# Kernel optimization log

Hardware: AMD Instinct MI355X
Metric: run time of the kernel (lower is better)

## Reference

```python
import jax, jax.numpy as jnp
import numpy as np

W_L1, W_NORMAL, W_LAPLACIAN = 1.0, 1.0, 0.1
NORM_EPS = 1e-6   # F.normalize eps
COS_EPS = 1e-8    # F.cosine_similarity default eps


def setup_inputs() -> dict:
    key = jax.random.key(0)
    k1, k2, k3, k4, k5, k6 = jax.random.split(key, 6)
    N, F, NNZ = 1_000_000, 2_000_000, 8_000_000
    return {
        "V_rec": jax.random.normal(k1, (N, 3), dtype=jnp.float32),
        "V_gt": jax.random.normal(k2, (N, 3), dtype=jnp.float32),
        "faces": jax.random.randint(k3, (F, 3), 0, N, dtype=jnp.int64)
        if jax.config.jax_enable_x64 else jax.random.randint(k3, (F, 3), 0, N, dtype=jnp.int32),
        "L_rows": jax.random.randint(k4, (NNZ,), 0, N, dtype=jnp.int32),
        "L_cols": jax.random.randint(k5, (NNZ,), 0, N, dtype=jnp.int32),
        "L_vals": jax.random.normal(k6, (NNZ,), dtype=jnp.float32),
    }


def _vertex_normals(verts, faces):
    # gather verts by face indices: [F,3] each
    v0 = verts[faces[:, 0]]
    v1 = verts[faces[:, 1]]
    v2 = verts[faces[:, 2]]
    face_normals = jnp.cross(v1 - v0, v2 - v0)  # [F,3]
    vn = (jnp.zeros_like(verts)
          .at[faces[:, 0]].add(face_normals)
          .at[faces[:, 1]].add(face_normals)
          .at[faces[:, 2]].add(face_normals))
    norm = jnp.linalg.norm(vn, axis=1, keepdims=True)
    return vn / jnp.maximum(norm, NORM_EPS)


def _cosine_sim(a, b):
    dot = jnp.sum(a * b, axis=1)
    na = jnp.linalg.norm(a, axis=1)
    nb = jnp.linalg.norm(b, axis=1)
    return dot / (jnp.maximum(na, COS_EPS) * jnp.maximum(nb, COS_EPS))


def _spmm(rows, cols, vals, V):
    # sparse [N,N] @ dense [N,3] via gather + segment_sum
    return jax.ops.segment_sum(vals[:, None] * V[cols], rows, num_segments=V.shape[0])


def reference(V_rec, V_gt, faces, L_rows, L_cols, L_vals):
    # L1 term
    loss_l1 = jnp.mean(jnp.abs(V_rec - V_gt))
    # Normal cosine term
    normals_gt = _vertex_normals(V_gt, faces)
    normals_rec = _vertex_normals(V_rec, faces)
    cos_n = jnp.nan_to_num(_cosine_sim(normals_rec, normals_gt), nan=1.0)
    loss_normal = jnp.mean(1.0 - cos_n)
    # Laplacian cosine term
    delta_gt = _spmm(L_rows, L_cols, L_vals, V_gt)
    delta_rec = _spmm(L_rows, L_cols, L_vals, V_rec)
    cos_l = jnp.nan_to_num(_cosine_sim(delta_rec, delta_gt), nan=1.0)
    loss_laplacian = jnp.mean(1.0 - cos_l)
    finite = jnp.isfinite(delta_gt).all() & jnp.isfinite(delta_rec).all()
    loss_laplacian = jnp.where(finite, loss_laplacian, 0.0)
    return W_L1 * loss_l1 + W_NORMAL * loss_normal + W_LAPLACIAN * loss_laplacian
```

## Files before the change

### kernel.cpp

```cpp
#include <hip/hip_runtime.h>
#include <hip/hip_bf16.h>

#define NORM_EPS_F 1e-6f
#define COS_EPS_F  1e-8f
#define BK   1024
#define BKSH 10

__device__ __forceinline__ void atomAddF(float* p, float v) {
    unsafeAtomicAdd(p, v);
}

template<int NV>
__device__ __forceinline__ void blockReduceAtomicN(float (&v)[NV], float* dst) {
    #pragma unroll
    for (int off = 32; off > 0; off >>= 1) {
        #pragma unroll
        for (int k = 0; k < NV; ++k) v[k] += __shfl_down(v[k], off, 64);
    }
    __shared__ float red[4][NV];
    int wave = threadIdx.x >> 6, lane = threadIdx.x & 63;
    if (lane == 0) {
        #pragma unroll
        for (int k = 0; k < NV; ++k) red[wave][k] = v[k];
    }
    __syncthreads();
    if (threadIdx.x == 0) {
        float s[NV];
        #pragma unroll
        for (int k = 0; k < NV; ++k) s[k] = 0.f;
        for (int w = 0; w < 4; ++w)
            #pragma unroll
            for (int k = 0; k < NV; ++k) s[k] += red[w][k];
        #pragma unroll
        for (int k = 0; k < NV; ++k) atomAddF(&dst[k], s[k]);
    }
}


__global__ void __launch_bounds__(256) pack_l1_kernel(
    const float* __restrict__ Vr, const float* __restrict__ Vg,
    float4* __restrict__ Vp, float* __restrict__ accum, int N)
{
    int i = blockIdx.x * blockDim.x + threadIdx.x;
    float l1[1] = {0.f};
    if (i < N) {
        float rx = Vr[3 * i], ry = Vr[3 * i + 1], rz = Vr[3 * i + 2];
        float gx = Vg[3 * i], gy = Vg[3 * i + 1], gz = Vg[3 * i + 2];
        Vp[2 * i]     = make_float4(rx, ry, rz, 0.f);
        Vp[2 * i + 1] = make_float4(gx, gy, gz, 0.f);
        l1[0] = fabsf(rx - gx) + fabsf(ry - gy) + fabsf(rz - gz);
    }
    blockReduceAtomicN<1>(l1, &accum[0]);
}

__global__ void __launch_bounds__(256) fn_kernel(
    const float4* __restrict__ Vp, const int* __restrict__ faces,
    float4* __restrict__ FN, int F)
{
    int f = blockIdx.x * blockDim.x + threadIdx.x;
    if (f >= F) return;
    int i0 = faces[3 * f], i1 = faces[3 * f + 1], i2 = faces[3 * f + 2];
    float4 r0 = Vp[2 * i0], r1 = Vp[2 * i1], r2 = Vp[2 * i2];
    float4 g0 = Vp[2 * i0 + 1], g1 = Vp[2 * i1 + 1], g2 = Vp[2 * i2 + 1];
    {
        float ax = r1.x - r0.x, ay = r1.y - r0.y, az = r1.z - r0.z;
        float bx = r2.x - r0.x, by = r2.y - r0.y, bz = r2.z - r0.z;
        FN[2 * f] = make_float4(ay * bz - az * by, az * bx - ax * bz, ax * by - ay * bx, 0.f);
    }
    {
        float ax = g1.x - g0.x, ay = g1.y - g0.y, az = g1.z - g0.z;
        float bx = g2.x - g0.x, by = g2.y - g0.y, bz = g2.z - g0.z;
        FN[2 * f + 1] = make_float4(ay * bz - az * by, az * bx - ax * bz, ax * by - ay * bx, 0.f);
    }
}

__global__ void __launch_bounds__(256) bucket_faces_kernel(
    const int* __restrict__ faces, int* __restrict__ cnt,
    unsigned* __restrict__ recF, int capF, int F, int b0, int bcnt, int chunk)
{
    __shared__ int hist[1024];
    int f0 = blockIdx.x * chunk;
    int f1 = min(f0 + chunk, F);
    for (int b = threadIdx.x; b < bcnt; b += blockDim.x) hist[b] = 0;
    __syncthreads();
    for (int f = f0 + threadIdx.x; f < f1; f += blockDim.x) {
        #pragma unroll
        for (int c = 0; c < 3; ++c) {
            unsigned bb = ((unsigned)faces[3 * f + c] >> BKSH) - (unsigned)b0;
            if (bb < (unsigned)bcnt) atomicAdd(&hist[bb], 1);
        }
    }
    __syncthreads();
    for (int b = threadIdx.x; b < bcnt; b += blockDim.x) {
        int h = hist[b];
        if (h) hist[b] = atomicAdd(&cnt[b], h);
    }
    __syncthreads();
    for (int f = f0 + threadIdx.x; f < f1; f += blockDim.x) {
        #pragma unroll
        for (int c = 0; c < 3; ++c) {
            int vtx = faces[3 * f + c];
            unsigned bb = ((unsigned)vtx >> BKSH) - (unsigned)b0;
            if (bb < (unsigned)bcnt) {
                int pos = atomicAdd(&hist[bb], 1);
                if (pos < capF)
                    recF[(size_t)bb * capF + pos] =
                        ((unsigned)f << BKSH) | (unsigned)(vtx & (BK - 1));
            }
        }
    }
}

__global__ void __launch_bounds__(256) accum_normals_kernel(
    const float4* __restrict__ Vp, const float4* __restrict__ FN,
    const int* __restrict__ faces,
    const int* __restrict__ cnt, const unsigned* __restrict__ recF, int capF,
    float* __restrict__ accum, int N, int b0, int use_fn)
{
    __shared__ float vnr[3 * BK];
    __shared__ float vng[3 * BK];
    int g = blockIdx.x;
    for (int i = threadIdx.x; i < 3 * BK; i += blockDim.x) { vnr[i] = 0.f; vng[i] = 0.f; }
    __syncthreads();

    int n = min(cnt[g], capF);
    for (int i = threadIdx.x; i < n; i += blockDim.x) {
        unsigned rec = recF[(size_t)g * capF + i];
        int lv = rec & (BK - 1);
        int f  = rec >> BKSH;
        float4 nr, ng;
        if (use_fn) {
            nr = FN[2 * f];
            ng = FN[2 * f + 1];
        } else {
            int i0 = faces[3 * f], i1 = faces[3 * f + 1], i2 = faces[3 * f + 2];
            float4 r0 = Vp[2 * i0], r1 = Vp[2 * i1], r2 = Vp[2 * i2];
            float4 g0 = Vp[2 * i0 + 1], g1 = Vp[2 * i1 + 1], g2 = Vp[2 * i2 + 1];
            float ax = r1.x - r0.x, ay = r1.y - r0.y, az = r1.z - r0.z;
            float bx = r2.x - r0.x, by = r2.y - r0.y, bz = r2.z - r0.z;
            nr = make_float4(ay * bz - az * by, az * bx - ax * bz, ax * by - ay * bx, 0.f);
            ax = g1.x - g0.x; ay = g1.y - g0.y; az = g1.z - g0.z;
            bx = g2.x - g0.x; by = g2.y - g0.y; bz = g2.z - g0.z;
            ng = make_float4(ay * bz - az * by, az * bx - ax * bz, ax * by - ay * bx, 0.f);
        }
        atomicAdd(&vnr[3 * lv + 0], nr.x);
        atomicAdd(&vnr[3 * lv + 1], nr.y);
        atomicAdd(&vnr[3 * lv + 2], nr.z);
        atomicAdd(&vng[3 * lv + 0], ng.x);
        atomicAdd(&vng[3 * lv + 1], ng.y);
        atomicAdd(&vng[3 * lv + 2], ng.z);
    }
    __syncthreads();

    float ln[1] = {0.f};
    for (int lv = threadIdx.x; lv < BK; lv += blockDim.x) {
        int gv = ((b0 + g) << BKSH) + lv;
        if (gv < N) {
            float ax = vnr[3 * lv], ay = vnr[3 * lv + 1], az = vnr[3 * lv + 2];
            float bx = vng[3 * lv], by = vng[3 * lv + 1], bz = vng[3 * lv + 2];
            float na = sqrtf(ax * ax + ay * ay + az * az);
            float nb = sqrtf(bx * bx + by * by + bz * bz);
            float ia = 1.0f / fmaxf(na, NORM_EPS_F);
            float ib = 1.0f / fmaxf(nb, NORM_EPS_F);
            ax *= ia; ay *= ia; az *= ia;
            bx *= ib; by *= ib; bz *= ib;
            float dot = ax * bx + ay * by + az * bz;
            float nna = sqrtf(ax * ax + ay * ay + az * az);
            float nnb = sqrtf(bx * bx + by * by + bz * bz);
            float cosn = dot / (fmaxf(nna, COS_EPS_F) * fmaxf(nnb, COS_EPS_F));
            if (isnan(cosn)) cosn = 1.0f;
            ln[0] += 1.0f - cosn;
        }
    }
    blockReduceAtomicN<1>(ln, &accum[1]);
}

__global__ void __launch_bounds__(256) bucket_L_kernel(
    const int* __restrict__ rows, const int* __restrict__ cols,
    const float* __restrict__ vals, int* __restrict__ cnt,
    int2* __restrict__ recL, int capL, int nnz, int b0, int bcnt, int chunk)
{
    __shared__ int hist[1024];
    int i0 = blockIdx.x * chunk;
    int i1 = min(i0 + chunk, nnz);
    for (int b = threadIdx.x; b < bcnt; b += blockDim.x) hist[b] = 0;
    __syncthreads();
    for (int i = i0 + threadIdx.x; i < i1; i += blockDim.x) {
        unsigned bb = ((unsigned)rows[i] >> BKSH) - (unsigned)b0;
        if (bb < (unsigned)bcnt) atomicAdd(&hist[bb], 1);
    }
    __syncthreads();
    for (int b = threadIdx.x; b < bcnt; b += blockDim.x) {
        int h = hist[b];
        if (h) hist[b] = atomicAdd(&cnt[b], h);
    }
    __syncthreads();
    for (int i = i0 + threadIdx.x; i < i1; i += blockDim.x) {
        int r = rows[i];
        unsigned bb = ((unsigned)r >> BKSH) - (unsigned)b0;
        if (bb < (unsigned)bcnt) {
            int pos = atomicAdd(&hist[bb], 1);
            if (pos < capL)
                recL[(size_t)bb * capL + pos] = make_int2(
                    (int)(((unsigned)cols[i] << BKSH) | (unsigned)(r & (BK - 1))),
                    __float_as_int(vals[i]));
        }
    }
}

__global__ void __launch_bounds__(256) accum_lap_kernel(
    const float4* __restrict__ Vp,
    const int* __restrict__ cnt, const int2* __restrict__ recL, int capL,
    float* __restrict__ accum, int N, int b0)
{
    __shared__ float dlr[3 * BK];
    __shared__ float dlg[3 * BK];
    int g = blockIdx.x;
    for (int i = threadIdx.x; i < 3 * BK; i += blockDim.x) { dlr[i] = 0.f; dlg[i] = 0.f; }
    __syncthreads();

    int n = min(cnt[g], capL);
    for (int i = threadIdx.x; i < n; i += blockDim.x) {
        int2 rc = recL[(size_t)g * capL + i];
        unsigned u = (unsigned)rc.x;
        int lv  = u & (BK - 1);
        int col = u >> BKSH;
        float v = __int_as_float(rc.y);
        float4 pr = Vp[2 * col];
        float4 pg = Vp[2 * col + 1];
        atomicAdd(&dlr[3 * lv + 0], v * pr.x);
        atomicAdd(&dlr[3 * lv + 1], v * pr.y);
        atomicAdd(&dlr[3 * lv + 2], v * pr.z);
        atomicAdd(&dlg[3 * lv + 0], v * pg.x);
        atomicAdd(&dlg[3 * lv + 1], v * pg.y);
        atomicAdd(&dlg[3 * lv + 2], v * pg.z);
    }
    __syncthreads();

    float vals2[2] = {0.f, 0.f};
    for (int lv = threadIdx.x; lv < BK; lv += blockDim.x) {
        int gv = ((b0 + g) << BKSH) + lv;
        if (gv < N) {
            float px = dlr[3 * lv], py = dlr[3 * lv + 1], pz = dlr[3 * lv + 2];
            float qx = dlg[3 * lv], qy = dlg[3 * lv + 1], qz = dlg[3 * lv + 2];
            bool fin = isfinite(px) && isfinite(py) && isfinite(pz) &&
                       isfinite(qx) && isfinite(qy) && isfinite(qz);
            vals2[1] += fin ? 0.f : 1.f;
            float dotl = px * qx + py * qy + pz * qz;
            float npn = sqrtf(px * px + py * py + pz * pz);
            float nqn = sqrtf(qx * qx + qy * qy + qz * qz);
            float cosl = dotl / (fmaxf(npn, COS_EPS_F) * fmaxf(nqn, COS_EPS_F));
            if (isnan(cosl)) cosl = 1.0f;
            vals2[0] += 1.0f - cosl;
        }
    }
    blockReduceAtomicN<2>(vals2, &accum[2]);
}

__global__ void finalize_kernel(const float* __restrict__ accum,
                                float* __restrict__ out, int N)
{
    float invN = 1.0f / (float)N;
    float l1 = accum[0] * invN * (1.0f / 3.0f);
    float ln = accum[1] * invN;
    float ll = (accum[3] > 0.0f) ? 0.0f : accum[2] * invN;
    out[0] = 1.0f * l1 + 1.0f * ln + 0.1f * ll;
}


__global__ void __launch_bounds__(256) face_normals_kernel(
    const float* __restrict__ Vr, const float* __restrict__ Vg,
    const int* __restrict__ faces,
    float* __restrict__ vn_rec, float* __restrict__ vn_gt, int F)
{
    int f = blockIdx.x * blockDim.x + threadIdx.x;
    if (f >= F) return;
    int i0 = faces[3 * f + 0], i1 = faces[3 * f + 1], i2 = faces[3 * f + 2];
    {
        float v0x = Vr[3 * i0], v0y = Vr[3 * i0 + 1], v0z = Vr[3 * i0 + 2];
        float v1x = Vr[3 * i1], v1y = Vr[3 * i1 + 1], v1z = Vr[3 * i1 + 2];
        float v2x = Vr[3 * i2], v2y = Vr[3 * i2 + 1], v2z = Vr[3 * i2 + 2];
        float ax = v1x - v0x, ay = v1y - v0y, az = v1z - v0z;
        float bx = v2x - v0x, by = v2y - v0y, bz = v2z - v0z;
        float nx = ay * bz - az * by, ny = az * bx - ax * bz, nz = ax * by - ay * bx;
        atomAddF(&vn_rec[3 * i0], nx); atomAddF(&vn_rec[3 * i0 + 1], ny); atomAddF(&vn_rec[3 * i0 + 2], nz);
        atomAddF(&vn_rec[3 * i1], nx); atomAddF(&vn_rec[3 * i1 + 1], ny); atomAddF(&vn_rec[3 * i1 + 2], nz);
        atomAddF(&vn_rec[3 * i2], nx); atomAddF(&vn_rec[3 * i2 + 1], ny); atomAddF(&vn_rec[3 * i2 + 2], nz);
    }
    {
        float v0x = Vg[3 * i0], v0y = Vg[3 * i0 + 1], v0z = Vg[3 * i0 + 2];
        float v1x = Vg[3 * i1], v1y = Vg[3 * i1 + 1], v1z = Vg[3 * i1 + 2];
        float v2x = Vg[3 * i2], v2y = Vg[3 * i2 + 1], v2z = Vg[3 * i2 + 2];
        float ax = v1x - v0x, ay = v1y - v0y, az = v1z - v0z;
        float bx = v2x - v0x, by = v2y - v0y, bz = v2z - v0z;
        float nx = ay * bz - az * by, ny = az * bx - ax * bz, nz = ax * by - ay * bx;
        atomAddF(&vn_gt[3 * i0], nx); atomAddF(&vn_gt[3 * i0 + 1], ny); atomAddF(&vn_gt[3 * i0 + 2], nz);
        atomAddF(&vn_gt[3 * i1], nx); atomAddF(&vn_gt[3 * i1 + 1], ny); atomAddF(&vn_gt[3 * i1 + 2], nz);
        atomAddF(&vn_gt[3 * i2], nx); atomAddF(&vn_gt[3 * i2 + 1], ny); atomAddF(&vn_gt[3 * i2 + 2], nz);
    }
}

__global__ void __launch_bounds__(256) spmm_kernel(
    const float* __restrict__ Vr, const float* __restrict__ Vg,
    const int* __restrict__ rows, const int* __restrict__ cols,
    const float* __restrict__ vals,
    float* __restrict__ dl_rec, float* __restrict__ dl_gt, int nnz)
{
    int i = blockIdx.x * blockDim.x + threadIdx.x;
    if (i >= nnz) return;
// ... 14 lines not shown
    float* __restrict__ accum, int N)
{
    int i = blockIdx.x * blockDim.x + threadIdx.x;
    float l1 = 0.0f, ln = 0.0f, ll = 0.0f, nonfin = 0.0f;
    if (i < N) {
        float rx = Vr[3 * i], ry = Vr[3 * i + 1], rz = Vr[3 * i + 2];
        float gx = Vg[3 * i], gy = Vg[3 * i + 1], gz = Vg[3 * i + 2];
        l1 = fabsf(rx - gx) + fabsf(ry - gy) + fabsf(rz - gz);
        float ax = vn_rec[3 * i], ay = vn_rec[3 * i + 1], az = vn_rec[3 * i + 2];
        float bx = vn_gt[3 * i],  by = vn_gt[3 * i + 1],  bz = vn_gt[3 * i + 2];
        float na = sqrtf(ax * ax + ay * ay + az * az);
        float nb = sqrtf(bx * bx + by * by + bz * bz);
        float ia = 1.0f / fmaxf(na, NORM_EPS_F);
        float ib = 1.0f / fmaxf(nb, NORM_EPS_F);
        ax *= ia; ay *= ia; az *= ia; bx *= ib; by *= ib; bz *= ib;
        float dot = ax * bx + ay * by + az * bz;
        float nna = sqrtf(ax * ax + ay * ay + az * az);
        float nnb = sqrtf(bx * bx + by * by + bz * bz);
        float cosn = dot / (fmaxf(nna, COS_EPS_F) * fmaxf(nnb, COS_EPS_F));
        if (isnan(cosn)) cosn = 1.0f;
        ln = 1.0f - cosn;
        float px = dl_rec[3 * i], py = dl_rec[3 * i + 1], pz = dl_rec[3 * i + 2];
        float qx = dl_gt[3 * i],  qy = dl_gt[3 * i + 1],  qz = dl_gt[3 * i + 2];
        bool fin = isfinite(px) && isfinite(py) && isfinite(pz) &&
                   isfinite(qx) && isfinite(qy) && isfinite(qz);
        nonfin = fin ? 0.0f : 1.0f;
        float dotl = px * qx + py * qy + pz * qz;
        float npn = sqrtf(px * px + py * py + pz * pz);
        float nqn = sqrtf(qx * qx + qy * qy + qz * qz);
        float cosl = dotl / (fmaxf(npn, COS_EPS_F) * fmaxf(nqn, COS_EPS_F));
        if (isnan(cosl)) cosl = 1.0f;
        ll = 1.0f - cosl;
    }
    float a[1] = {l1};  blockReduceAtomicN<1>(a, &accum[0]);
    float b[1] = {ln};  blockReduceAtomicN<1>(b, &accum[1]);
    float c2[2] = {ll, nonfin}; blockReduceAtomicN<2>(c2, &accum[2]);
}


extern "C" void kernel_launch(void* const* d_in, const int* in_sizes, int n_in,
                              void* d_out, int out_size, void* d_ws, size_t ws_size,
                              hipStream_t stream)
{
    const float* Vr    = (const float*)d_in[0];
    const float* Vg    = (const float*)d_in[1];
    const int*   faces = (const int*)d_in[2];
    const int*   Lr    = (const int*)d_in[3];
    const int*   Lc    = (const int*)d_in[4];
    const float* Lv    = (const float*)d_in[5];

    const int N   = in_sizes[0] / 3;
    const int F   = in_sizes[2] / 3;
    const int NNZ = in_sizes[3];
    const int NB  = (N + BK - 1) >> BKSH;

    float* ws = (float*)d_ws;
    const int B = 256;

    const long long baseW  = 1028;
    const long long vpackW = 8LL * N;
    const long long fnW    = 8LL * F;
    const long long totW   = (long long)(ws_size / 4);

    const int capF = 3 * F / (NB > 0 ? NB : 1) + 1 + 1024;
    const int capL = NNZ / (NB > 0 ? NB : 1) + 1 + 1024;

    long long availA = totW - baseW - vpackW - fnW;
    long long availB = totW - baseW - vpackW;
    bool tierA = availA >= (long long)capF * 64;
    long long availF = tierA ? availA : availB;

    int NBG_F = (int)(availF / capF);
    int NBG_L = (int)(availB / (2LL * capL));
    if (NBG_F > NB) NBG_F = NB;
    if (NBG_L > NB) NBG_L = NB;
    if (NBG_F > 1024) NBG_F = 1024;
    if (NBG_L > 1024) NBG_L = 1024;

    bool fast = (N <= (1 << 20)) && (F <= (1 << 22)) &&
                NBG_F >= 32 && NBG_L >= 32;

    if (fast) {
        float*    accum = ws;
        int*      cnt   = (int*)(ws + 4);
        float4*   Vp    = (float4*)(ws + baseW);
        float4*   FN    = (float4*)(ws + baseW + vpackW);
        unsigned* recF  = (unsigned*)(ws + baseW + vpackW + (tierA ? fnW : 0));
        int2*     recL  = (int2*)(ws + baseW + vpackW);

        hipMemsetAsync(accum, 0, 4 * sizeof(float), stream);

        pack_l1_kernel<<<dim3((N + B - 1) / B), dim3(B), 0, stream>>>(Vr, Vg, Vp, accum, N);
        if (tierA)
            fn_kernel<<<dim3((F + B - 1) / B), dim3(B), 0, stream>>>(Vp, faces, FN, F);

        const int CHF = 4096, CHL = 8192;
        int passF = (NB + NBG_F - 1) / NBG_F;
        for (int p = 0; p < passF; ++p) {
            int b0 = p * NBG_F;
            int bcnt = NB - b0 < NBG_F ? NB - b0 : NBG_F;
            hipMemsetAsync(cnt, 0, (size_t)bcnt * sizeof(int), stream);
            bucket_faces_kernel<<<dim3((F + CHF - 1) / CHF), dim3(B), 0, stream>>>(
                faces, cnt, recF, capF, F, b0, bcnt, CHF);
            accum_normals_kernel<<<dim3(bcnt), dim3(B), 0, stream>>>(
                Vp, FN, faces, cnt, recF, capF, accum, N, b0, tierA ? 1 : 0);
        }
        int passL = (NB + NBG_L - 1) / NBG_L;
        for (int p = 0; p < passL; ++p) {
            int b0 = p * NBG_L;
            int bcnt = NB - b0 < NBG_L ? NB - b0 : NBG_L;
            hipMemsetAsync(cnt, 0, (size_t)bcnt * sizeof(int), stream);
            bucket_L_kernel<<<dim3((NNZ + CHL - 1) / CHL), dim3(B), 0, stream>>>(
                Lr, Lc, Lv, cnt, recL, capL, NNZ, b0, bcnt, CHL);
            accum_lap_kernel<<<dim3(bcnt), dim3(B), 0, stream>>>(
                Vp, cnt, recL, capL, accum, N, b0);
        }
        finalize_kernel<<<dim3(1), dim3(1), 0, stream>>>(accum, (float*)d_out, N);
    } else {
        float* vn_rec = ws;
        float* vn_gt  = ws + (size_t)3 * N;
        float* dl_rec = ws + (size_t)6 * N;
        float* dl_gt  = ws + (size_t)9 * N;
        float* accum  = ws + (size_t)12 * N;
        hipMemsetAsync(d_ws, 0, ((size_t)12 * N + 4) * sizeof(float), stream);
        face_normals_kernel<<<dim3((F + B - 1) / B), dim3(B), 0, stream>>>(Vr, Vg, faces, vn_rec, vn_gt, F);
        spmm_kernel<<<dim3((NNZ + B - 1) / B), dim3(B), 0, stream>>>(Vr, Vg, Lr, Lc, Lv, dl_rec, dl_gt, NNZ);
        reduce_kernel<<<dim3((N + B - 1) / B), dim3(B), 0, stream>>>(Vr, Vg, vn_rec, vn_gt, dl_rec, dl_gt, accum, N);
        finalize_kernel<<<dim3(1), dim3(1), 0, stream>>>(accum, (float*)d_out, N);
    }
}
```

Baseline: 1.102 ms.

## Halve bucket size, batch gathers for memory-level parallelism, two faces per thread

Result: slower. 1.146 ms (+4.0%).

```diff
diff --git a/kernel.cpp b/kernel.cpp
--- a/kernel.cpp
+++ b/kernel.cpp
@@ -3,8 +3,9 @@
 
 #define NORM_EPS_F 1e-6f
 #define COS_EPS_F  1e-8f
-#define BK   1024
-#define BKSH 10
+#define BK   512
+#define BKSH 9
+#define NBGMAX 2048
 
 __device__ __forceinline__ void atomAddF(float* p, float v) {
     unsafeAtomicAdd(p, v);
@@ -57,20 +58,39 @@
     const float4* __restrict__ Vp, const int* __restrict__ faces,
     float4* __restrict__ FN, int F)
 {
-    int f = blockIdx.x * blockDim.x + threadIdx.x;
-    if (f >= F) return;
-    int i0 = faces[3 * f], i1 = faces[3 * f + 1], i2 = faces[3 * f + 2];
-    float4 r0 = Vp[2 * i0], r1 = Vp[2 * i1], r2 = Vp[2 * i2];
-    float4 g0 = Vp[2 * i0 + 1], g1 = Vp[2 * i1 + 1], g2 = Vp[2 * i2 + 1];
-    {
-        float ax = r1.x - r0.x, ay = r1.y - r0.y, az = r1.z - r0.z;
-        float bx = r2.x - r0.x, by = r2.y - r0.y, bz = r2.z - r0.z;
-        FN[2 * f] = make_float4(ay * bz - az * by, az * bx - ax * bz, ax * by - ay * bx, 0.f);
-    }
-    {
-        float ax = g1.x - g0.x, ay = g1.y - g0.y, az = g1.z - g0.z;
-        float bx = g2.x - g0.x, by = g2.y - g0.y, bz = g2.z - g0.z;
-        FN[2 * f + 1] = make_float4(ay * bz - az * by, az * bx - ax * bz, ax * by - ay * bx, 0.f);
+    int half = (F + 1) >> 1;
+    int t = blockIdx.x * blockDim.x + threadIdx.x;
+    if (t >= half) return;
+    int fi[2] = {t, t + half};
+    int n = (fi[1] < F) ? 2 : 1;
+    int idx[2][3];
+    #pragma unroll
+    for (int k = 0; k < 2; ++k) {
+        if (k < n) {
+            idx[k][0] = faces[3 * fi[k]];
+            idx[k][1] = faces[3 * fi[k] + 1];
+            idx[k][2] = faces[3 * fi[k] + 2];
+        }
+    }
+    float4 r0[2], r1[2], r2[2], g0[2], g1[2], g2[2];
+    #pragma unroll
+    for (int k = 0; k < 2; ++k) {
+        if (k < n) {
+            r0[k] = Vp[2 * idx[k][0]]; g0[k] = Vp[2 * idx[k][0] + 1];
+            r1[k] = Vp[2 * idx[k][1]]; g1[k] = Vp[2 * idx[k][1] + 1];
+            r2[k] = Vp[2 * idx[k][2]]; g2[k] = Vp[2 * idx[k][2] + 1];
+        }
+    }
+    #pragma unroll
+    for (int k = 0; k < 2; ++k) {
+        if (k < n) {
+            float ax = r1[k].x - r0[k].x, ay = r1[k].y - r0[k].y, az = r1[k].z - r0[k].z;
+            float bx = r2[k].x - r0[k].x, by = r2[k].y - r0[k].y, bz = r2[k].z - r0[k].z;
+            FN[2 * fi[k]] = make_float4(ay * bz - az * by, az * bx - ax * bz, ax * by - ay * bx, 0.f);
+            ax = g1[k].x - g0[k].x; ay = g1[k].y - g0[k].y; az = g1[k].z - g0[k].z;
+            bx = g2[k].x - g0[k].x; by = g2[k].y - g0[k].y; bz = g2[k].z - g0[k].z;
+            FN[2 * fi[k] + 1] = make_float4(ay * bz - az * by, az * bx - ax * bz, ax * by - ay * bx, 0.f);
+        }
     }
 }
 
@@ -78,7 +98,7 @@
     const int* __restrict__ faces, int* __restrict__ cnt,
     unsigned* __restrict__ recF, int capF, int F, int b0, int bcnt, int chunk)
 {
-    __shared__ int hist[1024];
+    __shared__ int hist[NBGMAX];
     int f0 = blockIdx.x * chunk;
     int f1 = min(f0 + chunk, F);
     for (int b = threadIdx.x; b < bcnt; b += blockDim.x) hist[b] = 0;
@@ -123,11 +143,36 @@
     for (int i = threadIdx.x; i < 3 * BK; i += blockDim.x) { vnr[i] = 0.f; vng[i] = 0.f; }
     __syncthreads();
 
+    const unsigned* rec = recF + (size_t)g * capF;
     int n = min(cnt[g], capF);
-    for (int i = threadIdx.x; i < n; i += blockDim.x) {
-        unsigned rec = recF[(size_t)g * capF + i];
-        int lv = rec & (BK - 1);
-        int f  = rec >> BKSH;
+    int i = threadIdx.x;
+    if (use_fn) {
+        for (; i + 768 < n; i += 1024) {
+            unsigned rc[4];
+            rc[0] = rec[i]; rc[1] = rec[i + 256]; rc[2] = rec[i + 512]; rc[3] = rec[i + 768];
+            float4 nr[4], ng[4];
+            #pragma unroll
+            for (int k = 0; k < 4; ++k) {
+                int f = rc[k] >> BKSH;
+                nr[k] = FN[2 * f];
+                ng[k] = FN[2 * f + 1];
+            }
+            #pragma unroll
+            for (int k = 0; k < 4; ++k) {
+                int lv = rc[k] & (BK - 1);
+                atomicAdd(&vnr[3 * lv + 0], nr[k].x);
+                atomicAdd(&vnr[3 * lv + 1], nr[k].y);
+                atomicAdd(&vnr[3 * lv + 2], nr[k].z);
+                atomicAdd(&vng[3 * lv + 0], ng[k].x);
+                atomicAdd(&vng[3 * lv + 1], ng[k].y);
+                atomicAdd(&vng[3 * lv + 2], ng[k].z);
+            }
+        }
+    }
+    for (; i < n; i += 256) {
+        unsigned rc = rec[i];
+        int lv = rc & (BK - 1);
+        int f  = rc >> BKSH;
         float4 nr, ng;
         if (use_fn) {
             nr = FN[2 * f];
@@ -180,7 +225,7 @@
     const float* __restrict__ vals, int* __restrict__ cnt,
     int2* __restrict__ recL, int capL, int nnz, int b0, int bcnt, int chunk)
 {
-    __shared__ int hist[1024];
+    __shared__ int hist[NBGMAX];
     int i0 = blockIdx.x * chunk;
     int i1 = min(i0 + chunk, nnz);
     for (int b = threadIdx.x; b < bcnt; b += blockDim.x) hist[b] = 0;
@@ -219,9 +264,33 @@
     for (int i = threadIdx.x; i < 3 * BK; i += blockDim.x) { dlr[i] = 0.f; dlg[i] = 0.f; }
     __syncthreads();
 
+    const int2* rec = recL + (size_t)g * capL;
     int n = min(cnt[g], capL);
-    for (int i = threadIdx.x; i < n; i += blockDim.x) {
-        int2 rc = recL[(size_t)g * capL + i];
+    int i = threadIdx.x;
+    for (; i + 768 < n; i += 1024) {
+        int2 rc[4];
+        rc[0] = rec[i]; rc[1] = rec[i + 256]; rc[2] = rec[i + 512]; rc[3] = rec[i + 768];
+        float4 pr[4], pg[4];
+        #pragma unroll
+        for (int k = 0; k < 4; ++k) {
+            int col = (unsigned)rc[k].x >> BKSH;
+            pr[k] = Vp[2 * col];
+            pg[k] = Vp[2 * col + 1];
+        }
+        #pragma unroll
+        for (int k = 0; k < 4; ++k) {
+            int lv = (unsigned)rc[k].x & (BK - 1);
+            float v = __int_as_float(rc[k].y);
+            atomicAdd(&dlr[3 * lv + 0], v * pr[k].x);
+            atomicAdd(&dlr[3 * lv + 1], v * pr[k].y);
+            atomicAdd(&dlr[3 * lv + 2], v * pr[k].z);
+            atomicAdd(&dlg[3 * lv + 0], v * pg[k].x);
+            atomicAdd(&dlg[3 * lv + 1], v * pg[k].y);
+            atomicAdd(&dlg[3 * lv + 2], v * pg[k].z);
+        }
+    }
+    for (; i < n; i += 256) {
+        int2 rc = rec[i];
         unsigned u = (unsigned)rc.x;
         int lv  = u & (BK - 1);
         int col = u >> BKSH;
@@ -380,13 +449,13 @@
     float* ws = (float*)d_ws;
     const int B = 256;
 
-    const long long baseW  = 1028;
+    const long long baseW  = 4 + NBGMAX;
     const long long vpackW = 8LL * N;
     const long long fnW    = 8LL * F;
     const long long totW   = (long long)(ws_size / 4);
 
-    const int capF = 3 * F / (NB > 0 ? NB : 1) + 1 + 1024;
-    const int capL = NNZ / (NB > 0 ? NB : 1) + 1 + 1024;
+    const int capF = 3 * F / (NB > 0 ? NB : 1) + 1 + 640;
+    const int capL = NNZ / (NB > 0 ? NB : 1) + 1 + 640;
 
     long long availA = totW - baseW - vpackW - fnW;
     long long availB = totW - baseW - vpackW;
@@ -397,8 +466,8 @@
     int NBG_L = (int)(availB / (2LL * capL));
     if (NBG_F > NB) NBG_F = NB;
     if (NBG_L > NB) NBG_L = NB;
-    if (NBG_F > 1024) NBG_F = 1024;
-    if (NBG_L > 1024) NBG_L = 1024;
+    if (NBG_F > NBGMAX) NBG_F = NBGMAX;
+    if (NBG_L > NBGMAX) NBG_L = NBGMAX;
 
     bool fast = (N <= (1 << 20)) && (F <= (1 << 22)) &&
                 NBG_F >= 32 && NBG_L >= 32;
@@ -414,8 +483,10 @@
         hipMemsetAsync(accum, 0, 4 * sizeof(float), stream);
 
         pack_l1_kernel<<<dim3((N + B - 1) / B), dim3(B), 0, stream>>>(Vr, Vg, Vp, accum, N);
-        if (tierA)
-            fn_kernel<<<dim3((F + B - 1) / B), dim3(B), 0, stream>>>(Vp, faces, FN, F);
+        if (tierA) {
+            int half = (F + 1) >> 1;
+            fn_kernel<<<dim3((half + B - 1) / B), dim3(B), 0, stream>>>(Vp, faces, FN, F);
+        }
 
         const int CHF = 4096, CHL = 8192;
         int passF = (NB + NBG_F - 1) / NBG_F;
```

## Replace per-pass bucketing with multi-level radix scatter and fp16-packed fat records

Applied to the files above, without the earlier changes.

Measured after the change: 1.394 ms. 26.5% more time.

```diff
diff --git a/kernel.cpp b/kernel.cpp
--- a/kernel.cpp
+++ b/kernel.cpp
@@ -1,13 +1,29 @@
 #include <hip/hip_runtime.h>
 #include <hip/hip_bf16.h>
+#include <hip/hip_fp16.h>
 
 #define NORM_EPS_F 1e-6f
 #define COS_EPS_F  1e-8f
-#define BK   1024
-#define BKSH 10
+#define BK    512
+#define BKSH  9
+#define CRSH  14
+#define K2    32
+#define CH1   4096
+#define CHFS  2048
 
 __device__ __forceinline__ void atomAddF(float* p, float v) {
     unsafeAtomicAdd(p, v);
+}
+
+__device__ __forceinline__ unsigned packh2(float a, float b) {
+    return (unsigned)__half_as_ushort(__float2half(a)) |
+           ((unsigned)__half_as_ushort(__float2half(b)) << 16);
+}
+__device__ __forceinline__ float unpL(int u) {
+    return __half2float(__ushort_as_half((unsigned short)((unsigned)u & 0xffff)));
+}
+__device__ __forceinline__ float unpH(int u) {
+    return __half2float(__ushort_as_half((unsigned short)((unsigned)u >> 16)));
 }
 
 template<int NV>
@@ -53,105 +69,186 @@
     blockReduceAtomicN<1>(l1, &accum[0]);
 }
 
-__global__ void __launch_bounds__(256) fn_kernel(
-    const float4* __restrict__ Vp, const int* __restrict__ faces,
-    float4* __restrict__ FN, int F)
-{
-    int f = blockIdx.x * blockDim.x + threadIdx.x;
-    if (f >= F) return;
-    int i0 = faces[3 * f], i1 = faces[3 * f + 1], i2 = faces[3 * f + 2];
-    float4 r0 = Vp[2 * i0], r1 = Vp[2 * i1], r2 = Vp[2 * i2];
-    float4 g0 = Vp[2 * i0 + 1], g1 = Vp[2 * i1 + 1], g2 = Vp[2 * i2 + 1];
+__global__ void __launch_bounds__(256) bucket_CL1(
+    const int* __restrict__ rows, const int* __restrict__ cols,
+    const float* __restrict__ vals,
+    int* __restrict__ cntC, int2* __restrict__ recA,
+    unsigned short* __restrict__ recS, int capC, int nnz, int chunk)
+{
+    __shared__ int hist[64];
+    int i0 = blockIdx.x * chunk, i1 = min(i0 + chunk, nnz);
+    if (threadIdx.x < 64) hist[threadIdx.x] = 0;
+    __syncthreads();
+    for (int i = i0 + threadIdx.x; i < i1; i += 256)
+        atomicAdd(&hist[(unsigned)cols[i] >> CRSH], 1);
+    __syncthreads();
+    if (threadIdx.x < 64) {
+        int h = hist[threadIdx.x];
+        if (h) hist[threadIdx.x] = atomicAdd(&cntC[threadIdx.x], h);
+    }
+    __syncthreads();
+    for (int i = i0 + threadIdx.x; i < i1; i += 256) {
+        unsigned c = (unsigned)cols[i];
+        int cb = c >> CRSH;
+        int pos = atomicAdd(&hist[cb], 1);
+        if (pos < capC) {
+            size_t idx = (size_t)cb * capC + pos;
+            recA[idx] = make_int2(rows[i], __float_as_int(vals[i]));
+            recS[idx] = (unsigned short)(c & ((1u << CRSH) - 1));
+        }
+    }
+}
+
+__global__ void __launch_bounds__(256) bucket_CL2(
+    const int* __restrict__ cntC, const int2* __restrict__ recA,
+    const unsigned short* __restrict__ recS, int capC,
+    int* __restrict__ cntS, int2* __restrict__ fineC, int capS,
+    int RPSH, int NP)
+{
+    __shared__ int hist[256];
+    int c = blockIdx.x;
+    int k = blockIdx.y;
+    int ch = (capC + K2 - 1) / K2;
+    int n = min(cntC[c], capC);
+    int i0 = k * ch, i1 = min(i0 + ch, n);
+    hist[threadIdx.x] = 0;
+    __syncthreads();
+    const size_t base = (size_t)c * capC;
+    for (int i = i0 + threadIdx.x; i < i1; i += 256) {
+        int key = ((int)((unsigned)recA[base + i].x >> RPSH) << 5) |
+                  ((unsigned)recS[base + i] >> 9);
+        atomicAdd(&hist[key], 1);
+    }
+    __syncthreads();
     {
-        float ax = r1.x - r0.x, ay = r1.y - r0.y, az = r1.z - r0.z;
-        float bx = r2.x - r0.x, by = r2.y - r0.y, bz = r2.z - r0.z;
-        FN[2 * f] = make_float4(ay * bz - az * by, az * bx - ax * bz, ax * by - ay * bx, 0.f);
-    }
-    {
-        float ax = g1.x - g0.x, ay = g1.y - g0.y, az = g1.z - g0.z;
-        float bx = g2.x - g0.x, by = g2.y - g0.y, bz = g2.z - g0.z;
-        FN[2 * f + 1] = make_float4(ay * bz - az * by, az * bx - ax * bz, ax * by - ay * bx, 0.f);
-    }
-}
-
-__global__ void __launch_bounds__(256) bucket_faces_kernel(
-    const int* __restrict__ faces, int* __restrict__ cnt,
-    unsigned* __restrict__ recF, int capF, int F, int b0, int bcnt, int chunk)
-{
-    __shared__ int hist[1024];
-    int f0 = blockIdx.x * chunk;
-    int f1 = min(f0 + chunk, F);
-    for (int b = threadIdx.x; b < bcnt; b += blockDim.x) hist[b] = 0;
-    __syncthreads();
-    for (int f = f0 + threadIdx.x; f < f1; f += blockDim.x) {
-        #pragma unroll
-        for (int c = 0; c < 3; ++c) {
-            unsigned bb = ((unsigned)faces[3 * f + c] >> BKSH) - (unsigned)b0;
-            if (bb < (unsigned)bcnt) atomicAdd(&hist[bb], 1);
-        }
-    }
-    __syncthreads();
-    for (int b = threadIdx.x; b < bcnt; b += blockDim.x) {
-        int h = hist[b];
-        if (h) hist[b] = atomicAdd(&cnt[b], h);
-    }
-    __syncthreads();
-    for (int f = f0 + threadIdx.x; f < f1; f += blockDim.x) {
-        #pragma unroll
-        for (int c = 0; c < 3; ++c) {
-            int vtx = faces[3 * f + c];
-            unsigned bb = ((unsigned)vtx >> BKSH) - (unsigned)b0;
-            if (bb < (unsigned)bcnt) {
-                int pos = atomicAdd(&hist[bb], 1);
-                if (pos < capF)
-                    recF[(size_t)bb * capF + pos] =
-                        ((unsigned)f << BKSH) | (unsigned)(vtx & (BK - 1));
+        int h = hist[threadIdx.x];
+        if (h) {
+            int s = (c * 32 + (threadIdx.x & 31)) * NP + (threadIdx.x >> 5);
+            hist[threadIdx.x] = atomicAdd(&cntS[s], h);
+        }
+    }
+    __syncthreads();
+    for (int i = i0 + threadIdx.x; i < i1; i += 256) {
+        int2 ra = recA[base + i];
+        unsigned rs = recS[base + i];
+        int key = ((int)((unsigned)ra.x >> RPSH) << 5) | (rs >> 9);
+        int pos = atomicAdd(&hist[key], 1);
+        if (pos < capS) {
+            int s = (c * 32 + (key & 31)) * NP + (key >> 5);
+            fineC[(size_t)s * capS + pos] =
+                make_int2((ra.x << 9) | (int)(rs & 511), ra.y);
+        }
+    }
+}
+
+__global__ void __launch_bounds__(256) lap_product(
+    const float4* __restrict__ Vp, const int* __restrict__ cntS,
+    const int2* __restrict__ fineC, int capS, int NP, int pass,
+    int* __restrict__ cntR, int4* __restrict__ fatR, int capRC,
+    int cbase, int N)
+{
+    __shared__ float4 vld[2 * BK];
+    __shared__ int2   stash[1024];
+    __shared__ int    hist[64];
+    int b = blockIdx.x;
+    int v0 = b << BKSH;
+    int lim = min(2 * BK, 2 * (N - v0));
+    for (int i = threadIdx.x; i < lim; i += 256)
+        vld[i] = Vp[2 * (size_t)v0 + i];
+    int s = b * NP + pass;
+    int n = min(cntS[s], capS);
+    const int2* rec = fineC + (size_t)s * capS;
+    for (int s0 = 0; s0 < n; s0 += 1024) {
+        int m = min(1024, n - s0);
+        __syncthreads();
+        if (threadIdx.x < 64) hist[threadIdx.x] = 0;
+        for (int i = threadIdx.x; i < m; i += 256) stash[i] = rec[s0 + i];
+        __syncthreads();
+        for (int i = threadIdx.x; i < m; i += 256)
+            atomicAdd(&hist[(((unsigned)stash[i].x >> 9) >> CRSH) - cbase], 1);
+        __syncthreads();
+        if (threadIdx.x < 64) {
+            int h = hist[threadIdx.x];
+            if (h) hist[threadIdx.x] = atomicAdd(&cntR[threadIdx.x], h);
+        }
+        __syncthreads();
+        for (int i = threadIdx.x; i < m; i += 256) {
+            int2 rc = stash[i];
+            int row = (int)((unsigned)rc.x >> 9);
+            int cl  = rc.x & (BK - 1);
+            int lc  = (row >> CRSH) - cbase;
+            int pos = atomicAdd(&hist[lc], 1);
+            if (pos < capRC) {
+                float v = __int_as_float(rc.y);
+                float4 vr = vld[2 * cl];
+                float4 vg = vld[2 * cl + 1];
+                fatR[(size_t)lc * capRC + pos] = make_int4(
+                    row,
+                    (int)packh2(v * vr.x, v * vr.y),
+                    (int)packh2(v * vr.z, v * vg.x),
+                    (int)packh2(v * vg.y, v * vg.z));
             }
         }
     }
 }
 
-__global__ void __launch_bounds__(256) accum_normals_kernel(
-    const float4* __restrict__ Vp, const float4* __restrict__ FN,
-    const int* __restrict__ faces,
-    const int* __restrict__ cnt, const unsigned* __restrict__ recF, int capF,
-    float* __restrict__ accum, int N, int b0, int use_fn)
-{
-    __shared__ float vnr[3 * BK];
-    __shared__ float vng[3 * BK];
-    int g = blockIdx.x;
-    for (int i = threadIdx.x; i < 3 * BK; i += blockDim.x) { vnr[i] = 0.f; vng[i] = 0.f; }
-    __syncthreads();
-
-    int n = min(cnt[g], capF);
-    for (int i = threadIdx.x; i < n; i += blockDim.x) {
-        unsigned rec = recF[(size_t)g * capF + i];
-        int lv = rec & (BK - 1);
-        int f  = rec >> BKSH;
-        float4 nr, ng;
-        if (use_fn) {
-            nr = FN[2 * f];
-            ng = FN[2 * f + 1];
-        } else {
-            int i0 = faces[3 * f], i1 = faces[3 * f + 1], i2 = faces[3 * f + 2];
-            float4 r0 = Vp[2 * i0], r1 = Vp[2 * i1], r2 = Vp[2 * i2];
-            float4 g0 = Vp[2 * i0 + 1], g1 = Vp[2 * i1 + 1], g2 = Vp[2 * i2 + 1];
-            float ax = r1.x - r0.x, ay = r1.y - r0.y, az = r1.z - r0.z;
-            float bx = r2.x - r0.x, by = r2.y - r0.y, bz = r2.z - r0.z;
-            nr = make_float4(ay * bz - az * by, az * bx - ax * bz, ax * by - ay * bx, 0.f);
-            ax = g1.x - g0.x; ay = g1.y - g0.y; az = g1.z - g0.z;
-            bx = g2.x - g0.x; by = g2.y - g0.y; bz = g2.z - g0.z;
-            ng = make_float4(ay * bz - az * by, az * bx - ax * bz, ax * by - ay * bx, 0.f);
-        }
-        atomicAdd(&vnr[3 * lv + 0], nr.x);
-        atomicAdd(&vnr[3 * lv + 1], nr.y);
-        atomicAdd(&vnr[3 * lv + 2], nr.z);
-        atomicAdd(&vng[3 * lv + 0], ng.x);
-        atomicAdd(&vng[3 * lv + 1], ng.y);
-        atomicAdd(&vng[3 * lv + 2], ng.z);
-    }
-    __syncthreads();
-
+__global__ void __launch_bounds__(256) refine_fat(
+    const int* __restrict__ cntIn, const int4* __restrict__ fatIn, int capIn,
+    int* __restrict__ cntOut, int4* __restrict__ fatOut, int capOut)
+{
+    __shared__ int hist[32];
+    int c = blockIdx.x;
+    int k = blockIdx.y;
+    int ch = (capIn + K2 - 1) / K2;
+    int n = min(cntIn[c], capIn);
+    int i0 = k * ch, i1 = min(i0 + ch, n);
+    if (threadIdx.x < 32) hist[threadIdx.x] = 0;
+    __syncthreads();
+    const size_t base = (size_t)c * capIn;
+    for (int i = i0 + threadIdx.x; i < i1; i += 256)
+        atomicAdd(&hist[((unsigned)fatIn[base + i].x >> BKSH) & 31], 1);
+    __syncthreads();
+    if (threadIdx.x < 32) {
+        int h = hist[threadIdx.x];
+        if (h) hist[threadIdx.x] = atomicAdd(&cntOut[c * 32 + threadIdx.x], h);
+    }
+    __syncthreads();
+    for (int i = i0 + threadIdx.x; i < i1; i += 256) {
+        int4 rc = fatIn[base + i];
+        int j = ((unsigned)rc.x >> BKSH) & 31;
+        int pos = atomicAdd(&hist[j], 1);
+        if (pos < capOut)
+            fatOut[(size_t)(c * 32 + j) * capOut + pos] = rc;
+    }
+}
+
+
+__device__ __forceinline__ void lap_epilogue(
+    const float* dlr, const float* dlg, float* accum, int N, int b0, int g)
+{
+    float vals2[2] = {0.f, 0.f};
+    for (int lv = threadIdx.x; lv < BK; lv += blockDim.x) {
+        int gv = ((b0 + g) << BKSH) + lv;
+        if (gv < N) {
+            float px = dlr[3 * lv], py = dlr[3 * lv + 1], pz = dlr[3 * lv + 2];
+            float qx = dlg[3 * lv], qy = dlg[3 * lv + 1], qz = dlg[3 * lv + 2];
+            bool fin = isfinite(px) && isfinite(py) && isfinite(pz) &&
+                       isfinite(qx) && isfinite(qy) && isfinite(qz);
+            vals2[1] += fin ? 0.f : 1.f;
+            float dotl = px * qx + py * qy + pz * qz;
+            float npn = sqrtf(px * px + py * py + pz * pz);
+            float nqn = sqrtf(qx * qx + qy * qy + qz * qz);
+            float cosl = dotl / (fmaxf(npn, COS_EPS_F) * fmaxf(nqn, COS_EPS_F));
+            if (isnan(cosl)) cosl = 1.0f;
+            vals2[0] += 1.0f - cosl;
+        }
+    }
+    blockReduceAtomicN<2>(vals2, &accum[2]);
+}
+
+__device__ __forceinline__ void normals_epilogue(
+    const float* vnr, const float* vng, float* accum, int N, int b0, int g)
+{
     float ln[1] = {0.f};
     for (int lv = threadIdx.x; lv < BK; lv += blockDim.x) {
         int gv = ((b0 + g) << BKSH) + lv;
@@ -175,86 +272,131 @@
     blockReduceAtomicN<1>(ln, &accum[1]);
 }
 
-__global__ void __launch_bounds__(256) bucket_L_kernel(
-    const int* __restrict__ rows, const int* __restrict__ cols,
-    const float* __restrict__ vals, int* __restrict__ cnt,
-    int2* __restrict__ recL, int capL, int nnz, int b0, int bcnt, int chunk)
-{
-    __shared__ int hist[1024];
-    int i0 = blockIdx.x * chunk;
-    int i1 = min(i0 + chunk, nnz);
-    for (int b = threadIdx.x; b < bcnt; b += blockDim.x) hist[b] = 0;
-    __syncthreads();
-    for (int i = i0 + threadIdx.x; i < i1; i += blockDim.x) {
-        unsigned bb = ((unsigned)rows[i] >> BKSH) - (unsigned)b0;
-        if (bb < (unsigned)bcnt) atomicAdd(&hist[bb], 1);
-    }
-    __syncthreads();
-    for (int b = threadIdx.x; b < bcnt; b += blockDim.x) {
-        int h = hist[b];
-        if (h) hist[b] = atomicAdd(&cnt[b], h);
-    }
-    __syncthreads();
-    for (int i = i0 + threadIdx.x; i < i1; i += blockDim.x) {
-        int r = rows[i];
-        unsigned bb = ((unsigned)r >> BKSH) - (unsigned)b0;
-        if (bb < (unsigned)bcnt) {
-            int pos = atomicAdd(&hist[bb], 1);
-            if (pos < capL)
-                recL[(size_t)bb * capL + pos] = make_int2(
-                    (int)(((unsigned)cols[i] << BKSH) | (unsigned)(r & (BK - 1))),
-                    __float_as_int(vals[i]));
-        }
-    }
-}
-
-__global__ void __launch_bounds__(256) accum_lap_kernel(
-    const float4* __restrict__ Vp,
-    const int* __restrict__ cnt, const int2* __restrict__ recL, int capL,
+
+__global__ void __launch_bounds__(256) accum_fat_lap(
+    const int* __restrict__ cntW, const int4* __restrict__ fat, int capOut,
     float* __restrict__ accum, int N, int b0)
 {
     __shared__ float dlr[3 * BK];
     __shared__ float dlg[3 * BK];
     int g = blockIdx.x;
-    for (int i = threadIdx.x; i < 3 * BK; i += blockDim.x) { dlr[i] = 0.f; dlg[i] = 0.f; }
-    __syncthreads();
-
-    int n = min(cnt[g], capL);
-    for (int i = threadIdx.x; i < n; i += blockDim.x) {
-        int2 rc = recL[(size_t)g * capL + i];
-        unsigned u = (unsigned)rc.x;
-        int lv  = u & (BK - 1);
-        int col = u >> BKSH;
-        float v = __int_as_float(rc.y);
-        float4 pr = Vp[2 * col];
-        float4 pg = Vp[2 * col + 1];
-        atomicAdd(&dlr[3 * lv + 0], v * pr.x);
-        atomicAdd(&dlr[3 * lv + 1], v * pr.y);
-        atomicAdd(&dlr[3 * lv + 2], v * pr.z);
-        atomicAdd(&dlg[3 * lv + 0], v * pg.x);
-        atomicAdd(&dlg[3 * lv + 1], v * pg.y);
-        atomicAdd(&dlg[3 * lv + 2], v * pg.z);
-    }
-    __syncthreads();
-
-    float vals2[2] = {0.f, 0.f};
-    for (int lv = threadIdx.x; lv < BK; lv += blockDim.x) {
-        int gv = ((b0 + g) << BKSH) + lv;
-        if (gv < N) {
-            float px = dlr[3 * lv], py = dlr[3 * lv + 1], pz = dlr[3 * lv + 2];
-            float qx = dlg[3 * lv], qy = dlg[3 * lv + 1], qz = dlg[3 * lv + 2];
-            bool fin = isfinite(px) && isfinite(py) && isfinite(pz) &&
-                       isfinite(qx) && isfinite(qy) && isfinite(qz);
-            vals2[1] += fin ? 0.f : 1.f;
-            float dotl = px * qx + py * qy + pz * qz;
-            float npn = sqrtf(px * px + py * py + pz * pz);
-            float nqn = sqrtf(qx * qx + qy * qy + qz * qz);
-            float cosl = dotl / (fmaxf(npn, COS_EPS_F) * fmaxf(nqn, COS_EPS_F));
-            if (isnan(cosl)) cosl = 1.0f;
-            vals2[0] += 1.0f - cosl;
-        }
-    }
-    blockReduceAtomicN<2>(vals2, &accum[2]);
+    for (int i = threadIdx.x; i < 3 * BK; i += 256) { dlr[i] = 0.f; dlg[i] = 0.f; }
+    __syncthreads();
+    int n = min(cntW[g], capOut);
+    const int4* rec = fat + (size_t)g * capOut;
+    for (int i = threadIdx.x; i < n; i += 256) {
+        int4 rc = rec[i];
+        int lv = rc.x & (BK - 1);
+        atomicAdd(&dlr[3 * lv + 0], unpL(rc.y));
+        atomicAdd(&dlr[3 * lv + 1], unpH(rc.y));
+        atomicAdd(&dlr[3 * lv + 2], unpL(rc.z));
+        atomicAdd(&dlg[3 * lv + 0], unpH(rc.z));
+        atomicAdd(&dlg[3 * lv + 1], unpL(rc.w));
+        atomicAdd(&dlg[3 * lv + 2], unpH(rc.w));
+    }
+    __syncthreads();
+    lap_epilogue(dlr, dlg, accum, N, b0, g);
+}
+
+__global__ void __launch_bounds__(256) accum_fat_norm(
+    const int* __restrict__ cntW, const int4* __restrict__ fat, int capOut,
+    float* __restrict__ accum, int N, int b0)
+{
+    __shared__ float vnr[3 * BK];
+    __shared__ float vng[3 * BK];
+    int g = blockIdx.x;
+    for (int i = threadIdx.x; i < 3 * BK; i += 256) { vnr[i] = 0.f; vng[i] = 0.f; }
+    __syncthreads();
+    int n = min(cntW[g], capOut);
+    const int4* rec = fat + (size_t)g * capOut;
+    for (int i = threadIdx.x; i < n; i += 256) {
+        int4 rc = rec[i];
+        int lv = rc.x & (BK - 1);
+        atomicAdd(&vnr[3 * lv + 0], unpL(rc.y));
+        atomicAdd(&vnr[3 * lv + 1], unpH(rc.y));
+        atomicAdd(&vnr[3 * lv + 2], unpL(rc.z));
+        atomicAdd(&vng[3 * lv + 0], unpH(rc.z));
+        atomicAdd(&vng[3 * lv + 1], unpL(rc.w));
+        atomicAdd(&vng[3 * lv + 2], unpH(rc.w));
+    }
+    __syncthreads();
+    normals_epilogue(vnr, vng, accum, N, b0, g);
+}
+
+__global__ void __launch_bounds__(256) fn_scatter(
+    const float4* __restrict__ Vp, const int* __restrict__ faces, int F,
+    int* __restrict__ cntN, int4* __restrict__ fatN, int capNC)
+{
+    __shared__ unsigned stash[3 * CHFS];
+    __shared__ int hist[64];
+    int f0 = blockIdx.x * CHFS;
+    int f1 = min(f0 + CHFS, F);
+    if (threadIdx.x < 64) hist[threadIdx.x] = 0;
+    __syncthreads();
+    for (int f = f0 + threadIdx.x; f < f1; f += 512) {
+        int fB = f + 256;
+        bool hasB = fB < f1;
+        int a0 = faces[3 * f], a1 = faces[3 * f + 1], a2 = faces[3 * f + 2];
+        int c0 = 0, c1 = 0, c2 = 0;
+        if (hasB) { c0 = faces[3 * fB]; c1 = faces[3 * fB + 1]; c2 = faces[3 * fB + 2]; }
+        float4 ar0 = Vp[2 * a0], ag0 = Vp[2 * a0 + 1];
+        float4 ar1 = Vp[2 * a1], ag1 = Vp[2 * a1 + 1];
+        float4 ar2 = Vp[2 * a2], ag2 = Vp[2 * a2 + 1];
+        float4 br0, bg0, br1, bg1, br2, bg2;
+        if (hasB) {
+            br0 = Vp[2 * c0]; bg0 = Vp[2 * c0 + 1];
+            br1 = Vp[2 * c1]; bg1 = Vp[2 * c1 + 1];
+            br2 = Vp[2 * c2]; bg2 = Vp[2 * c2 + 1];
+        }
+        {
+            float ax = ar1.x - ar0.x, ay = ar1.y - ar0.y, az = ar1.z - ar0.z;
+            float bx = ar2.x - ar0.x, by = ar2.y - ar0.y, bz = ar2.z - ar0.z;
+            float nrx = ay * bz - az * by, nry = az * bx - ax * bz, nrz = ax * by - ay * bx;
+            ax = ag1.x - ag0.x; ay = ag1.y - ag0.y; az = ag1.z - ag0.z;
+            bx = ag2.x - ag0.x; by = ag2.y - ag0.y; bz = ag2.z - ag0.z;
+            float ngx = ay * bz - az * by, ngy = az * bx - ax * bz, ngz = ax * by - ay * bx;
+            int li = f - f0;
+            stash[3 * li]     = packh2(nrx, nry);
+            stash[3 * li + 1] = packh2(nrz, ngx);
+            stash[3 * li + 2] = packh2(ngy, ngz);
+            atomicAdd(&hist[(unsigned)a0 >> CRSH], 1);
+            atomicAdd(&hist[(unsigned)a1 >> CRSH], 1);
+            atomicAdd(&hist[(unsigned)a2 >> CRSH], 1);
+        }
+        if (hasB) {
+            float ax = br1.x - br0.x, ay = br1.y - br0.y, az = br1.z - br0.z;
+            float bx = br2.x - br0.x, by = br2.y - br0.y, bz = br2.z - br0.z;
+            float nrx = ay * bz - az * by, nry = az * bx - ax * bz, nrz = ax * by - ay * bx;
+            ax = bg1.x - bg0.x; ay = bg1.y - bg0.y; az = bg1.z - bg0.z;
+            bx = bg2.x - bg0.x; by = bg2.y - bg0.y; bz = bg2.z - bg0.z;
+            float ngx = ay * bz - az * by, ngy = az * bx - ax * bz, ngz = ax * by - ay * bx;
+            int li = fB - f0;
+            stash[3 * li]     = packh2(nrx, nry);
+            stash[3 * li + 1] = packh2(nrz, ngx);
+            stash[3 * li + 2] = packh2(ngy, ngz);
+            atomicAdd(&hist[(unsigned)c0 >> CRSH], 1);
+            atomicAdd(&hist[(unsigned)c1 >> CRSH], 1);
+            atomicAdd(&hist[(unsigned)c2 >> CRSH], 1);
+        }
+    }
+    __syncthreads();
+    if (threadIdx.x < 64) {
+        int h = hist[threadIdx.x];
+        if (h) hist[threadIdx.x] = atomicAdd(&cntN[threadIdx.x], h);
+    }
+    __syncthreads();
+    for (int f = f0 + threadIdx.x; f < f1; f += 256) {
+        int li = f - f0;
+        int s0 = (int)stash[3 * li], s1 = (int)stash[3 * li + 1], s2 = (int)stash[3 * li + 2];
+        #pragma unroll
+        for (int c = 0; c < 3; ++c) {
+            int v = faces[3 * f + c];
+            int cb = (unsigned)v >> CRSH;
+            int pos = atomicAdd(&hist[cb], 1);
+            if (pos < capNC)
+                fatN[(size_t)cb * capNC + pos] = make_int4(v, s0, s1, s2);
+        }
+    }
 }
 
 __global__ void finalize_kernel(const float* __restrict__ accum,
@@ -375,68 +517,112 @@
     const int N   = in_sizes[0] / 3;
     const int F   = in_sizes[2] / 3;
     const int NNZ = in_sizes[3];
-    const int NB  = (N + BK - 1) >> BKSH;
+    const int NBF = (N + BK - 1) >> BKSH;
+    const int NCC = (NBF + 31) >> 5;
 
     float* ws = (float*)d_ws;
     const int B = 256;
 
-    const long long baseW  = 1028;
-    const long long vpackW = 8LL * N;
-    const long long fnW    = 8LL * F;
     const long long totW   = (long long)(ws_size / 4);
-
-    const int capF = 3 * F / (NB > 0 ? NB : 1) + 1 + 1024;
-    const int capL = NNZ / (NB > 0 ? NB : 1) + 1 + 1024;
-
-    long long availA = totW - baseW - vpackW - fnW;
-    long long availB = totW - baseW - vpackW;
-    bool tierA = availA >= (long long)capF * 64;
-    long long availF = tierA ? availA : availB;
-
-    int NBG_F = (int)(availF / capF);
-    int NBG_L = (int)(availB / (2LL * capL));
-    if (NBG_F > NB) NBG_F = NB;
-    if (NBG_L > NB) NBG_L = NB;
-    if (NBG_F > 1024) NBG_F = 1024;
-    if (NBG_L > 1024) NBG_L = 1024;
-
-    bool fast = (N <= (1 << 20)) && (F <= (1 << 22)) &&
-                NBG_F >= 32 && NBG_L >= 32;
+    const long long fixedW = 4 + 64 + 2048 + 16384;
+    const long long vpW    = 8LL * N;
+
+    const long long capC  = NNZ / 64 + NNZ / 1024 + 512;
+    const long long Xw    = 64 * capC * 2 + (64 * capC + 1) / 2;
+    const long long capRC = NNZ / 64 + NNZ / 512 + 1024;
+    const long long capRS = NNZ / (NBF > 0 ? NBF : 1) + NNZ / (8LL * (NBF > 0 ? NBF : 1)) + 256;
+    const long long capNC = 3LL * F / 64 + 3LL * F / 512 + 1024;
+    const long long NRw   = 64 * capNC * 4;
+    const long long capNS = 3LL * F / (NBF > 0 ? NBF : 1) + 3LL * F / (8LL * (NBF > 0 ? NBF : 1)) + 256;
+
+    int bppL = 0, bppN = 0;
+    long long capSL = 0;
+    long long arena = 0;
+    const int cand[4] = {2048, 1024, 512, 256};
+    for (int li = 0; li < 4 && bppL == 0; ++li) {
+        int bl = cand[li];
+        int np = (NBF + bl - 1) / bl;
+        if (np > 8) continue;
+        long long cS = NNZ / ((long long)NBF * np) + NNZ / (4LL * NBF * np) + 128;
+        long long Yw = (long long)NBF * np * cS * 2;
+        long long Zw = (long long)(bl >> 5) * capRC * 4;
+        long long Ww = (long long)bl * capRS * 4;
+        long long lapA = Xw + Yw + Zw + (Ww <= Xw ? 0 : Ww);
+        for (int ni = 0; ni < 4; ++ni) {
+            int bn = cand[ni];
+            long long NFw = (long long)bn * capNS * 4;
+            long long normA = NRw + NFw;
+            long long ar = lapA > normA ? lapA : normA;
+            if (fixedW + vpW + ar <= totW) {
+                bppL = bl; bppN = bn; capSL = cS; arena = ar;
+                break;
+            }
+        }
+    }
+
+    bool fast = (N <= (1 << 20)) && (F <= (1 << 22)) && NBF >= 64 && bppL > 0;
 
     if (fast) {
-        float*    accum = ws;
-        int*      cnt   = (int*)(ws + 4);
-        float4*   Vp    = (float4*)(ws + baseW);
-        float4*   FN    = (float4*)(ws + baseW + vpackW);
-        unsigned* recF  = (unsigned*)(ws + baseW + vpackW + (tierA ? fnW : 0));
-        int2*     recL  = (int2*)(ws + baseW + vpackW);
-
-        hipMemsetAsync(accum, 0, 4 * sizeof(float), stream);
+        const int NP  = (NBF + bppL - 1) / bppL;
+        const int NPn = (NBF + bppN - 1) / bppN;
+        int RPSH = BKSH;
+        { int t = bppL; while (t > 1) { t >>= 1; ++RPSH; } }
+
+        float* accum  = ws;
+        int*   cnt64  = (int*)(ws + 4);
+        int*   cntW   = (int*)(ws + 68);
+        int*   cntS   = (int*)(ws + 2116);
+        float4* Vp    = (float4*)(ws + fixedW);
+        float* arenaP = ws + fixedW + vpW;
+
+        long long cS = capSL;
+        long long Yw = (long long)NBF * NP * cS * 2;
+        long long Zw = (long long)(bppL >> 5) * capRC * 4;
+        long long Ww = (long long)bppL * capRS * 4;
+        int2*           recA  = (int2*)arenaP;
+        unsigned short* recS  = (unsigned short*)(arenaP + 64 * capC * 2);
+        int2*           fineC = (int2*)(arenaP + Xw);
+        int4*           fatR  = (int4*)(arenaP + Xw + Yw);
+        int4*           fatW  = (Ww <= Xw) ? (int4*)arenaP : (int4*)(arenaP + Xw + Yw + Zw);
+        int4*           fatNR = (int4*)arenaP;
+        int4*           fatNF = (int4*)(arenaP + NRw);
+
+        hipMemsetAsync(ws, 0, fixedW * sizeof(float), stream);
 
         pack_l1_kernel<<<dim3((N + B - 1) / B), dim3(B), 0, stream>>>(Vr, Vg, Vp, accum, N);
-        if (tierA)
-            fn_kernel<<<dim3((F + B - 1) / B), dim3(B), 0, stream>>>(Vp, faces, FN, F);
-
-        const int CHF = 4096, CHL = 8192;
-        int passF = (NB + NBG_F - 1) / NBG_F;
-        for (int p = 0; p < passF; ++p) {
-            int b0 = p * NBG_F;
-            int bcnt = NB - b0 < NBG_F ? NB - b0 : NBG_F;
-            hipMemsetAsync(cnt, 0, (size_t)bcnt * sizeof(int), stream);
-            bucket_faces_kernel<<<dim3((F + CHF - 1) / CHF), dim3(B), 0, stream>>>(
-                faces, cnt, recF, capF, F, b0, bcnt, CHF);
-            accum_normals_kernel<<<dim3(bcnt), dim3(B), 0, stream>>>(
-                Vp, FN, faces, cnt, recF, capF, accum, N, b0, tierA ? 1 : 0);
-        }
-        int passL = (NB + NBG_L - 1) / NBG_L;
-        for (int p = 0; p < passL; ++p) {
-            int b0 = p * NBG_L;
-            int bcnt = NB - b0 < NBG_L ? NB - b0 : NBG_L;
-            hipMemsetAsync(cnt, 0, (size_t)bcnt * sizeof(int), stream);
-            bucket_L_kernel<<<dim3((NNZ + CHL - 1) / CHL), dim3(B), 0, stream>>>(
-                Lr, Lc, Lv, cnt, recL, capL, NNZ, b0, bcnt, CHL);
-            accum_lap_kernel<<<dim3(bcnt), dim3(B), 0, stream>>>(
-                Vp, cnt, recL, capL, accum, N, b0);
+
+        bucket_CL1<<<dim3((NNZ + CH1 - 1) / CH1), dim3(B), 0, stream>>>(
+            Lr, Lc, Lv, cnt64, recA, recS, (int)capC, NNZ, CH1);
+        bucket_CL2<<<dim3(NCC, K2), dim3(B), 0, stream>>>(
+            cnt64, recA, recS, (int)capC, cntS, fineC, (int)cS, RPSH, NP);
+        for (int p = 0; p < NP; ++p) {
+            int cbase = p * (bppL >> 5);
+            int nCPp = NCC - cbase; if (nCPp > (bppL >> 5)) nCPp = bppL >> 5;
+            if (nCPp <= 0) break;
+            int bcnt = NBF - p * bppL; if (bcnt > bppL) bcnt = bppL;
+            hipMemsetAsync(ws + 4, 0, 2112 * sizeof(int), stream);
+            lap_product<<<dim3(NBF), dim3(B), 0, stream>>>(
+                Vp, cntS, fineC, (int)cS, NP, p, cnt64, fatR, (int)capRC, cbase, N);
+            refine_fat<<<dim3(nCPp, K2), dim3(B), 0, stream>>>(
+                cnt64, fatR, (int)capRC, cntW, fatW, (int)capRS);
+            accum_fat_lap<<<dim3(bcnt), dim3(B), 0, stream>>>(
+                cntW, fatW, (int)capRS, accum, N, p * bppL);
+        }
+
+        hipMemsetAsync(ws + 4, 0, 2112 * sizeof(int), stream);
+        fn_scatter<<<dim3((F + CHFS - 1) / CHFS), dim3(B), 0, stream>>>(
+            Vp, faces, F, cnt64, fatNR, (int)capNC);
+        for (int p = 0; p < NPn; ++p) {
+            int cbase = p * (bppN >> 5);
+            int nCPn = NCC - cbase; if (nCPn > (bppN >> 5)) nCPn = bppN >> 5;
+            if (nCPn <= 0) break;
+            int bcnt = NBF - p * bppN; if (bcnt > bppN) bcnt = bppN;
+            if (p > 0) hipMemsetAsync(ws + 68, 0, 2048 * sizeof(int), stream);
+            refine_fat<<<dim3(nCPn, K2), dim3(B), 0, stream>>>(
+                cnt64 + cbase, fatNR + (size_t)cbase * capNC, (int)capNC,
+                cntW, fatNF, (int)capNS);
+            accum_fat_norm<<<dim3(bcnt), dim3(B), 0, stream>>>(
+                cntW, fatNF, (int)capNS, accum, N, p * bppN);
         }
         finalize_kernel<<<dim3(1), dim3(1), 0, stream>>>(accum, (float*)d_out, N);
     } else {
```
